# Performance work log

Hardware: AMD Instinct MI355X
Metric: run time of the kernel (lower is better)

Reference implementation:

```python
import jax, jax.numpy as jnp
import numpy as np

H = 16       # num_attention_heads
HKV = 4      # num_key_value_heads
G = H // HKV # num_kv_groups
D = 128      # head_dim
ROT = 64     # rotary dim = head_dim * rope_partial_rotary_factor (0.5)
BLK = 64     # sparse_block_size
LOCAL = 8    # sparse_local_num_blocks
GLOB = 1     # sparse_global_num_blocks
SCALE = 1.0 / float(np.sqrt(D))
NEG = -1000000000.0


def _rotate_half(x):
    x1, x2 = x[..., : x.shape[-1] // 2], x[..., x.shape[-1] // 2 :]
    return jnp.concatenate((-x2, x1), axis=-1)


def _sparse_tables(n_blocks):
    """Static numpy tables mirroring _get_sparse_tables + causal masking.
    Returns idx (n,S) int32 gather table and mask (n, BLK, S, BLK) bool (True = masked)."""
    S = LOCAL + GLOB
    idx = np.zeros((n_blocks, S), np.int32)
    valid = np.zeros((n_blocks, S), bool)
    for i in range(n_blocks):
        sel = [g for g in range(GLOB) if g < n_blocks]
        sel += list(range(max(0, i - (LOCAL - 1)), i + 1))
        li = list(dict.fromkeys(sel))  # dedupe, keep order
        idx[i, : len(li)] = li
        valid[i, : len(li)] = True
    ii = np.arange(n_blocks)[:, None]
    dead = (~valid) | (idx > ii)          # invalid slot or future block
    selfb = idx == ii                     # diagonal block -> intra-causal
    jq = np.arange(BLK)[:, None]
    jk = np.arange(BLK)[None, :]
    intra = jk > jq                       # (q, k) strictly-upper masked
    mask = dead[:, None, :, None] | (selfb[:, None, :, None] & intra[None, :, None, :])
    return idx, mask                      # (n,S), (n,BLK,S,BLK)


def setup_inputs() -> dict:
    key = jax.random.key(0)
    ks = jax.random.split(key, 6)
    B_, T, HID = 2, 4096, 2048
    hidden_states = jax.random.normal(ks[0], (B_, T, HID), dtype=jnp.float32)
    # real RoPE tables for the rotary sub-dim
    inv_freq = 1.0 / (10000.0 ** (np.arange(0, ROT, 2, dtype=np.float32) / ROT))
    freqs = np.arange(T, dtype=np.float32)[:, None] * inv_freq[None, :]
    emb = np.concatenate([freqs, freqs], axis=-1)  # (T, ROT)
    cos = jnp.broadcast_to(jnp.asarray(np.cos(emb)), (B_, T, ROT))
    sin = jnp.broadcast_to(jnp.asarray(np.sin(emb)), (B_, T, ROT))
    Wq = jax.random.normal(ks[1], (H * D, HID), dtype=jnp.float32) * 0.02
    Wk = jax.random.normal(ks[2], (HKV * D, HID), dtype=jnp.float32) * 0.02
    Wv = jax.random.normal(ks[3], (HKV * D, HID), dtype=jnp.float32) * 0.02
    Wo = jax.random.normal(ks[4], (HID, H * D), dtype=jnp.float32) * 0.02
    return {"hidden_states": hidden_states, "cos": cos, "sin": sin,
            "Wq": Wq, "Wk": Wk, "Wv": Wv, "Wo": Wo}


def reference(hidden_states, cos, sin, Wq, Wk, Wv, Wo):
    B_, T, _ = hidden_states.shape
    q = (hidden_states @ Wq.T).reshape(B_, T, H, D).transpose(0, 2, 1, 3)    # (b,H,T,D)
    k = (hidden_states @ Wk.T).reshape(B_, T, HKV, D).transpose(0, 2, 1, 3)  # (b,HKV,T,D)
    v = (hidden_states @ Wv.T).reshape(B_, T, HKV, D).transpose(0, 2, 1, 3)
    # partial RoPE on first ROT dims
    c = cos[:, None, :, :]
    s = sin[:, None, :, :]
    def rope(x):
        xr, xp = x[..., :ROT], x[..., ROT:]
        xr = xr * c + _rotate_half(xr) * s
        return jnp.concatenate([xr, xp], axis=-1)
    q, k = rope(q), rope(k)
    # block-sparse local+global attention (prefill, T multiple of BLK)
    n = T // BLK
    idx_np, mask_np = _sparse_tables(n)
    idx = jnp.asarray(idx_np)
    mask = jnp.asarray(mask_np)  # (n, BLKq, S, BLKk)
    qb = q.reshape(B_, HKV, G, n, BLK, D)
    kb = k.reshape(B_, HKV, n, BLK, D)
    vb = v.reshape(B_, HKV, n, BLK, D)
    ksel = kb[:, :, idx]  # (b,HKV,n,S,BLK,D)
    vsel = vb[:, :, idx]
    scores = jnp.einsum('bhgnqd,bhnskd->bhgnqsk',
                        qb.astype(jnp.float32), ksel.astype(jnp.float32)) * SCALE
    scores = jnp.where(mask[None, None, None], NEG, scores)
    sh = scores.shape
    probs = jax.nn.softmax(scores.reshape(*sh[:5], -1), axis=-1).reshape(sh)
    out = jnp.einsum('bhgnqsk,bhnskd->bhgnqd', probs, vsel.astype(jnp.float32))
    out = out.astype(hidden_states.dtype).reshape(B_, H, T, D)
    out = out.transpose(0, 2, 1, 3).reshape(B_, T, H * D)
    return out @ Wo.T
```

## Files before the change

### kernel.cpp

```cpp
#include <hip/hip_runtime.h>
#include <hip/hip_bf16.h>

#define Hq   16
#define HKV  4
#define Dh   128
#define ROT  64
#define BLKQ 64
#define NBLK 64
#define Tlen 4096
#define Bsz  2
#define HID  2048
#define QKVC 3072
#define SCALE_C 0.08838834764831845f

typedef __attribute__((ext_vector_type(8))) short bf16x8;
typedef __attribute__((ext_vector_type(4))) float f32x4;

#define MFMA16(a, b, c) __builtin_amdgcn_mfma_f32_16x16x32_bf16((a), (b), (c), 0, 0, 0)

__device__ __forceinline__ void async_copy16(__hip_bfloat16* lds, const __hip_bfloat16* g) {
    __builtin_amdgcn_global_load_lds(
        (const __attribute__((address_space(1))) void*)g,
        (__attribute__((address_space(3))) void*)lds,
        16, 0, 0);
}

__global__ __launch_bounds__(256) void cvt_kernel(
    const float* __restrict__ s0, const float* __restrict__ s1,
    const float* __restrict__ s2, const float* __restrict__ s3,
    const float* __restrict__ s4,
    __hip_bfloat16* __restrict__ base,
    int n0, int n1, int n2, int n3, int n4)
{
    const float* src;
    size_t off, n;
    switch (blockIdx.y) {
        case 0:  src = s0; off = 0;                          n = n0; break;
        case 1:  src = s1; off = (size_t)n0;                 n = n1; break;
        case 2:  src = s2; off = (size_t)n0 + n1;            n = n2; break;
        case 3:  src = s3; off = (size_t)n0 + n1 + n2;       n = n3; break;
        default: src = s4; off = (size_t)n0 + n1 + n2 + n3;  n = n4; break;
    }
    __hip_bfloat16* dst = base + off;
    const size_t stride = (size_t)gridDim.x * 2048;
    for (size_t i = ((size_t)blockIdx.x * 256 + threadIdx.x) * 8; i < n; i += stride) {
        const float4 a = *(const float4*)(src + i);
        const float4 b = *(const float4*)(src + i + 4);
        union { bf16x8 v; __hip_bfloat16 e[8]; } u;
        u.e[0] = __float2bfloat16(a.x); u.e[1] = __float2bfloat16(a.y);
        u.e[2] = __float2bfloat16(a.z); u.e[3] = __float2bfloat16(a.w);
        u.e[4] = __float2bfloat16(b.x); u.e[5] = __float2bfloat16(b.y);
        u.e[6] = __float2bfloat16(b.z); u.e[7] = __float2bfloat16(b.w);
        *(bf16x8*)(dst + i) = u.v;
    }
}

template <bool ROPE_, bool F32OUT>
__global__ __launch_bounds__(256, 2) void gemm128db(
    const __hip_bfloat16* __restrict__ A,
    const __hip_bfloat16* __restrict__ B0,
    const __hip_bfloat16* __restrict__ B1,
    const __hip_bfloat16* __restrict__ B2,
    int n1c, int n2c,
    void* __restrict__ C,
    int M, int N, int K,
    const float* __restrict__ cosb,
    const float* __restrict__ sinb)
{
    __shared__ __align__(16) __hip_bfloat16 As[2][128 * 64];
    __shared__ __align__(16) __hip_bfloat16 Bs[2][128 * 64];

    const int m0 = blockIdx.y * 128;
    const int n0 = blockIdx.x * 128;
    const __hip_bfloat16* Bp;
    int nb;
    if (n0 < n1c)      { Bp = B0; nb = n0; }
    else if (n0 < n2c) { Bp = B1; nb = n0 - n1c; }
    else               { Bp = B2; nb = n0 - n2c; }

    const int tid  = threadIdx.x;
    const int lane = tid & 63;
    const int w    = tid >> 6;
    const int wm   = (w >> 1) * 64;
    const int wn   = (w & 1) * 64;
    const int lr   = lane >> 3;
    const int lc   = lane & 7;
    const int m16  = lane & 15;
    const int q8   = lane >> 4;
    const int NT   = K >> 6;

    f32x4 acc[4][4] = {};

    auto stageA = [&](int buf, int kc) {
        #pragma unroll
        for (int ii = 0; ii < 4; ++ii) {
            const int r8 = w * 32 + ii * 8;
            const int r  = r8 + lr;
            const int cg = lc ^ (r & 7);
            async_copy16(&As[buf][r8 * 64], A + (size_t)(m0 + r) * K + kc + cg * 8);
        }
    };
    auto stageB = [&](int buf, int kc) {
        #pragma unroll
        for (int ii = 0; ii < 4; ++ii) {
            const int r8 = w * 32 + ii * 8;
            const int r  = r8 + lr;
            const int cg = lc ^ (r & 7);
            async_copy16(&Bs[buf][r8 * 64], Bp + (size_t)(nb + r) * K + kc + cg * 8);
        }
    };

    stageA(0, 0);
    stageB(0, 0);
    stageA(1, 64);
    stageB(1, 64);
    asm volatile("s_waitcnt vmcnt(8)" ::: "memory");
    __builtin_amdgcn_s_barrier();

    for (int u = 0; u < NT; ++u) {
        const int P  = u & 1;
        const __hip_bfloat16* Ap_ = As[P];
        const __hip_bfloat16* Bq_ = Bs[P];

        bf16x8 a0[4], b0[4], a1[4], b1[4];
        #pragma unroll
        for (int t = 0; t < 4; ++t) {
            const int row = wm + t * 16 + m16;
            const int col = wn + t * 16 + m16;
            a0[t] = *(const bf16x8*)&Ap_[row * 64 + ((q8)     ^ (row & 7)) * 8];
            b0[t] = *(const bf16x8*)&Bq_[col * 64 + ((q8)     ^ (col & 7)) * 8];
            a1[t] = *(const bf16x8*)&Ap_[row * 64 + ((4 + q8) ^ (row & 7)) * 8];
            b1[t] = *(const bf16x8*)&Bq_[col * 64 + ((4 + q8) ^ (col & 7)) * 8];
        }
        asm volatile("s_waitcnt lgkmcnt(0)" ::: "memory");
        __builtin_amdgcn_sched_barrier(0);
        __builtin_amdgcn_s_barrier();
        __builtin_amdgcn_sched_barrier(0);

        if (u + 2 < NT) {
            stageA(P, (u + 2) << 6);
            stageB(P, (u + 2) << 6);
        }

        __builtin_amdgcn_s_setprio(1);
        #pragma unroll
        for (int i = 0; i < 4; ++i)
            #pragma unroll
            for (int j = 0; j < 4; ++j)
                acc[i][j] = MFMA16(a0[i], b0[j], acc[i][j]);
        #pragma unroll
        for (int i = 0; i < 4; ++i)
            #pragma unroll
            for (int j = 0; j < 4; ++j)
                acc[i][j] = MFMA16(a1[i], b1[j], acc[i][j]);
        __builtin_amdgcn_s_setprio(0);

        if (u + 2 < NT) {
            asm volatile("s_waitcnt vmcnt(8)" ::: "memory");
        } else {
            asm volatile("s_waitcnt vmcnt(0)" ::: "memory");
        }
        __builtin_amdgcn_s_barrier();
    }

    if (ROPE_ && n0 < n2c && wn == 0) {
        #pragma unroll
        for (int i = 0; i < 4; ++i)
            #pragma unroll
            for (int r = 0; r < 4; ++r) {
                const int bt = m0 + wm + i * 16 + q8 * 4 + r;
                #pragma unroll
                for (int j = 0; j < 2; ++j) {
                    const int d = j * 16 + m16;
                    const float c = cosb[(size_t)bt * ROT + d];
                    const float s = sinb[(size_t)bt * ROT + d];
                    const float x1 = acc[i][j][r];
                    const float x2 = acc[i][j + 2][r];
                    acc[i][j][r]     = x1 * c - x2 * s;
                    acc[i][j + 2][r] = x2 * c + x1 * s;
                }
            }
    }

    #pragma unroll
    for (int i = 0; i < 4; ++i)
        #pragma unroll
        for (int j = 0; j < 4; ++j)
            #pragma unroll
            for (int r = 0; r < 4; ++r) {
                const int row = m0 + wm + i * 16 + q8 * 4 + r;
                const int col = n0 + wn + j * 16 + m16;
                if (F32OUT)
                    ((float*)C)[(size_t)row * N + col] = acc[i][j][r];
                else
                    ((__hip_bfloat16*)C)[(size_t)row * N + col] =
                        __float2bfloat16(acc[i][j][r]);
            }
}

__global__ __launch_bounds__(256) void vtrans_kernel(
    const __hip_bfloat16* __restrict__ qkv,
    __hip_bfloat16* __restrict__ vtg)
{
    const int tb = blockIdx.x;
    const int pr = blockIdx.y;
    const __hip_bfloat16* src =
        qkv + ((size_t)(pr >> 2) * Tlen + tb * 64) * QKVC + HID + 512 + (pr & 3) * Dh;
    __hip_bfloat16* dst = vtg + (size_t)pr * Dh * Tlen + tb * 64;
    const int tid = threadIdx.x;
    #pragma unroll
    for (int t2 = 0; t2 < 4; ++t2) {
        const int c  = tid + t2 * 256;
        const int d  = c >> 3;
        const int t0 = (c & 7) * 8;
        union { bf16x8 v; __hip_bfloat16 e[8]; } u;
        #pragma unroll
        for (int j = 0; j < 8; ++j)
            u.e[j] = src[(size_t)(t0 + j) * QKVC + d];
        *(bf16x8*)(dst + (size_t)d * Tlen + t0) = u.v;
    }
}

__global__ __launch_bounds__(256, 3) void attn_kernel(
    const __hip_bfloat16* __restrict__ qkv,
    const __hip_bfloat16* __restrict__ vtg,
    __hip_bfloat16* __restrict__ outb)
{
    const int i   = blockIdx.x;
    const int h   = blockIdx.y;
    const int b   = blockIdx.z;
    const int kvh = h >> 2;
    const int tid  = threadIdx.x;
    const int lane = tid & 63;
    const int w    = tid >> 6;
    const int m16  = lane & 15;
    const int q8   = lane >> 4;

    __shared__ __align__(16) __hip_bfloat16 Ks[64 * 136];
    __shared__ __align__(16) __hip_bfloat16 VT[128 * 72];
    __shared__ __align__(16) __hip_bfloat16 Pb[4][16 * 72];

    bf16x8 qf[4];
    {
        const __hip_bfloat16* qp =
            qkv + (size_t)(b * Tlen + i * BLKQ + w * 16 + m16) * QKVC + h * Dh + q8 * 8;
        for (int ks = 0; ks < 4; ++ks) qf[ks] = *(const bf16x8*)(qp + ks * 32);
    }

    f32x4 o[8] = {};
    float mrow[4] = {-1e30f, -1e30f, -1e30f, -1e30f};
    float lrow[4] = {0.f, 0.f, 0.f, 0.f};

    const int nsel = (i + 1 < 9) ? (i + 1) : 9;
    auto kb_of = [&](int j) { return (i <= 7) ? j : ((j == 0) ? 0 : (i - 8 + j)); };

    const __hip_bfloat16* vtbase = vtg + (size_t)(b * HKV + kvh) * Dh * Tlen;

    bf16x8 kr[4], vr[4];
    {
        const int kb0 = kb_of(0);
        const __hip_bfloat16* kbase =
            qkv + (size_t)(b * Tlen + kb0 * BLKQ) * QKVC + HID + kvh * Dh;
        #pragma unroll
        for (int t = 0; t < 4; ++t) {
            const int c = tid + t * 256;
            kr[t] = *(const bf16x8*)(kbase + (size_t)(c >> 4) * QKVC + (c & 15) * 8);
            vr[t] = *(const bf16x8*)(vtbase + (size_t)(c >> 3) * Tlen
                                     + kb0 * BLKQ + (c & 7) * 8);
        }
    }

    for (int j = 0; j < nsel; ++j) {
        const int kb = kb_of(j);

        __syncthreads();
        #pragma unroll
        for (int t = 0; t < 4; ++t) {
            const int c = tid + t * 256;
            *(bf16x8*)&Ks[(c >> 4) * 136 + (c & 15) * 8] = kr[t];
        }
        #pragma unroll
        for (int t = 0; t < 4; ++t) {
            const int c = tid + t * 256;
            *(bf16x8*)&VT[(c >> 3) * 72 + (c & 7) * 8] = vr[t];
        }
        __syncthreads();

        if (j + 1 < nsel) {
            const int kbn = kb_of(j + 1);
            const __hip_bfloat16* kbase =
                qkv + (size_t)(b * Tlen + kbn * BLKQ) * QKVC + HID + kvh * Dh;
            #pragma unroll
            for (int t = 0; t < 4; ++t) {
                const int c = tid + t * 256;
                kr[t] = *(const bf16x8*)(kbase + (size_t)(c >> 4) * QKVC + (c & 15) * 8);
                vr[t] = *(const bf16x8*)(vtbase + (size_t)(c >> 3) * Tlen
                                         + kbn * BLKQ + (c & 7) * 8);
            }
        }

        float sv[4][4];
        __builtin_amdgcn_s_setprio(1);
        for (int nt = 0; nt < 4; ++nt) {
            f32x4 s = {0.f, 0.f, 0.f, 0.f};
            for (int ks = 0; ks < 4; ++ks) {
                bf16x8 kf = *(const bf16x8*)&Ks[(nt * 16 + m16) * 136 + ks * 32 + q8 * 8];
                s = MFMA16(qf[ks], kf, s);
            }
            for (int r = 0; r < 4; ++r) sv[nt][r] = s[r] * SCALE_C;
        }
        __builtin_amdgcn_s_setprio(0);
        if (kb == i) {
            for (int nt = 0; nt < 4; ++nt) {
                const int key = nt * 16 + m16;
                for (int r = 0; r < 4; ++r) {
                    const int qr = w * 16 + q8 * 4 + r;
                    if (key > qr) sv[nt][r] = -1e9f;
                }
            }
        }

        float alpha[4];
        for (int r = 0; r < 4; ++r) {
            float mx = fmaxf(fmaxf(sv[0][r], sv[1][r]), fmaxf(sv[2][r], sv[3][r]));
            for (int off = 1; off < 16; off <<= 1) mx = fmaxf(mx, __shfl_xor(mx, off, 64));
            const float newm = fmaxf(mrow[r], mx);
            alpha[r] = __expf(mrow[r] - newm);
            mrow[r] = newm;
            float rs = 0.f;
            for (int nt = 0; nt < 4; ++nt) {
                const float p = __expf(sv[nt][r] - newm);
                sv[nt][r] = p;
                rs += p;
            }
            for (int off = 1; off < 16; off <<= 1) rs += __shfl_xor(rs, off, 64);
            lrow[r] = lrow[r] * alpha[r] + rs;
        }

        __hip_bfloat16* Pw = &Pb[w][0];
        for (int nt = 0; nt < 4; ++nt)
            for (int r = 0; r < 4; ++r)
                Pw[(q8 * 4 + r) * 72 + nt * 16 + m16] = __float2bfloat16(sv[nt][r]);

        for (int dt = 0; dt < 8; ++dt)
            for (int r = 0; r < 4; ++r)
                o[dt][r] *= alpha[r];

        asm volatile("s_waitcnt lgkmcnt(0)" ::: "memory");
        __builtin_amdgcn_sched_barrier(0);

        __builtin_amdgcn_s_setprio(1);
        for (int kk = 0; kk < 2; ++kk) {
            bf16x8 pf = *(const bf16x8*)&Pw[m16 * 72 + kk * 32 + q8 * 8];
            for (int dt = 0; dt < 8; ++dt) {
                bf16x8 vf = *(const bf16x8*)&VT[(dt * 16 + m16) * 72 + kk * 32 + q8 * 8];
                o[dt] = MFMA16(pf, vf, o[dt]);
            }
        }
        __builtin_amdgcn_s_setprio(0);
    }

    float rcp[4];
    for (int r = 0; r < 4; ++r) rcp[r] = 1.0f / lrow[r];
    __hip_bfloat16* op = outb + (size_t)(b * Tlen + i * BLKQ) * (Hq * Dh) + h * Dh;
    for (int dt = 0; dt < 8; ++dt)
        for (int r = 0; r < 4; ++r) {
            const float val = o[dt][r] * rcp[r];
            op[(size_t)(w * 16 + q8 * 4 + r) * (Hq * Dh) + dt * 16 + m16] =
                __float2bfloat16(val);
        }
}

extern "C" void kernel_launch(void* const* d_in, const int* in_sizes, int n_in,
                              void* d_out, int out_size, void* d_ws, size_t ws_size,
                              hipStream_t stream) {
    const float* hs   = (const float*)d_in[0];
    const float* cosb = (const float*)d_in[1];
    const float* sinb = (const float*)d_in[2];
    const float* Wq   = (const float*)d_in[3];
    const float* Wk   = (const float*)d_in[4];
    const float* Wv   = (const float*)d_in[5];
    const float* Wo   = (const float*)d_in[6];

    const int M = Bsz * Tlen;
    const int nHS = M * HID;
    const int nWq = Hq * Dh * HID;
    const int nWk = HKV * Dh * HID;
    const int nWv = nWk;
    const int nWo = HID * Hq * Dh;

    __hip_bfloat16* hsb  = (__hip_bfloat16*)d_ws;
    __hip_bfloat16* wqb  = hsb + nHS;
    __hip_bfloat16* wkb  = wqb + nWq;
    __hip_bfloat16* wvb  = wkb + nWk;
    __hip_bfloat16* wob  = wvb + nWv;
    __hip_bfloat16* qkv  = wob + nWo;
    __hip_bfloat16* attn = qkv + (size_t)M * QKVC;
    __hip_bfloat16* vtg  = attn + (size_t)M * (Hq * Dh);

    cvt_kernel<<<dim3(8192, 5), 256, 0, stream>>>(
        hs, Wq, Wk, Wv, Wo, hsb, nHS, nWq, nWk, nWv, nWo);
    gemm128db<true, false><<<dim3(QKVC / 128, M / 128), 256, 0, stream>>>(
        hsb, wqb, wkb, wvb, HID, HID + 512, qkv, M, QKVC, HID, cosb, sinb);
    vtrans_kernel<<<dim3(NBLK, Bsz * HKV), 256, 0, stream>>>(qkv, vtg);
    attn_kernel<<<dim3(NBLK, Hq, Bsz), 256, 0, stream>>>(qkv, vtg, attn);
    gemm128db<false, true><<<dim3(HID / 128, M / 128), 256, 0, stream>>>(
        attn, wob, wob, wob, HID, HID, d_out, M, HID, HID, nullptr, nullptr);
}
```

Baseline: 415.8 us.

## Transpose attention MFMA operands so each lane owns one query row

Swaps the A/B operands of both MFMAs so the accumulator is transposed. Each lane now holds a single query row, which cuts the softmax max and sum reductions from four 16-lane shuffle trees to two shuffles per row. P is written to LDS as packed 4-element vectors and the output as 8-byte stores. VT and P tiles switch from padded rows to an XOR-swizzled layout to avoid bank conflicts without padding. This reduces shuffle and LDS traffic, with some risk of a wrong swizzle or layout mismatch.

Measured after the change: 413.6 us. Within noise of the previous version (-0.5%).

```diff
diff --git a/kernel.cpp b/kernel.cpp
--- a/kernel.cpp
+++ b/kernel.cpp
@@ -15,6 +15,7 @@
 
 typedef __attribute__((ext_vector_type(8))) short bf16x8;
 typedef __attribute__((ext_vector_type(4))) float f32x4;
+typedef __attribute__((ext_vector_type(4))) unsigned short u16x4;
 
 #define MFMA16(a, b, c) __builtin_amdgcn_mfma_f32_16x16x32_bf16((a), (b), (c), 0, 0, 0)
 
@@ -237,8 +238,8 @@
     const int q8   = lane >> 4;
 
     __shared__ __align__(16) __hip_bfloat16 Ks[64 * 136];
-    __shared__ __align__(16) __hip_bfloat16 VT[128 * 72];
-    __shared__ __align__(16) __hip_bfloat16 Pb[4][16 * 72];
+    __shared__ __align__(16) __hip_bfloat16 VT[128 * 64];
+    __shared__ __align__(16) __hip_bfloat16 Pb[4][16 * 64];
 
     bf16x8 qf[4];
     {
@@ -248,8 +249,7 @@
     }
 
     f32x4 o[8] = {};
-    float mrow[4] = {-1e30f, -1e30f, -1e30f, -1e30f};
-    float lrow[4] = {0.f, 0.f, 0.f, 0.f};
+    float mrow = -1e30f, lrow = 0.f;
 
     const int nsel = (i + 1 < 9) ? (i + 1) : 9;
     auto kb_of = [&](int j) { return (i <= 7) ? j : ((j == 0) ? 0 : (i - 8 + j)); };
@@ -282,7 +282,8 @@
         #pragma unroll
         for (int t = 0; t < 4; ++t) {
             const int c = tid + t * 256;
-            *(bf16x8*)&VT[(c >> 3) * 72 + (c & 7) * 8] = vr[t];
+            const int row = c >> 3;
+            *(bf16x8*)&VT[row * 64 + (((c & 7) ^ (row & 7)) << 3)] = vr[t];
         }
         __syncthreads();
 
@@ -305,70 +306,88 @@
             f32x4 s = {0.f, 0.f, 0.f, 0.f};
             for (int ks = 0; ks < 4; ++ks) {
                 bf16x8 kf = *(const bf16x8*)&Ks[(nt * 16 + m16) * 136 + ks * 32 + q8 * 8];
-                s = MFMA16(qf[ks], kf, s);
+                s = MFMA16(kf, qf[ks], s);
             }
             for (int r = 0; r < 4; ++r) sv[nt][r] = s[r] * SCALE_C;
         }
         __builtin_amdgcn_s_setprio(0);
         if (kb == i) {
-            for (int nt = 0; nt < 4; ++nt) {
-                const int key = nt * 16 + m16;
-                for (int r = 0; r < 4; ++r) {
-                    const int qr = w * 16 + q8 * 4 + r;
-                    if (key > qr) sv[nt][r] = -1e9f;
-                }
-            }
-        }
-
-        float alpha[4];
-        for (int r = 0; r < 4; ++r) {
-            float mx = fmaxf(fmaxf(sv[0][r], sv[1][r]), fmaxf(sv[2][r], sv[3][r]));
-            for (int off = 1; off < 16; off <<= 1) mx = fmaxf(mx, __shfl_xor(mx, off, 64));
-            const float newm = fmaxf(mrow[r], mx);
-            alpha[r] = __expf(mrow[r] - newm);
-            mrow[r] = newm;
-            float rs = 0.f;
-            for (int nt = 0; nt < 4; ++nt) {
+            const int qr = w * 16 + m16;
+            #pragma unroll
+            for (int nt = 0; nt < 4; ++nt)
+                #pragma unroll
+                for (int r = 0; r < 4; ++r)
+                    if (nt * 16 + q8 * 4 + r > qr) sv[nt][r] = -1e9f;
+        }
+
+        float mx = sv[0][0];
+        #pragma unroll
+        for (int nt = 0; nt < 4; ++nt)
+            #pragma unroll
+            for (int r = 0; r < 4; ++r) mx = fmaxf(mx, sv[nt][r]);
+        mx = fmaxf(mx, __shfl_xor(mx, 16, 64));
+        mx = fmaxf(mx, __shfl_xor(mx, 32, 64));
+        const float newm = fmaxf(mrow, mx);
+        const float alpha = __expf(mrow - newm);
+        mrow = newm;
+        float rs = 0.f;
+        #pragma unroll
+        for (int nt = 0; nt < 4; ++nt)
+            #pragma unroll
+            for (int r = 0; r < 4; ++r) {
                 const float p = __expf(sv[nt][r] - newm);
                 sv[nt][r] = p;
                 rs += p;
             }
-            for (int off = 1; off < 16; off <<= 1) rs += __shfl_xor(rs, off, 64);
-            lrow[r] = lrow[r] * alpha[r] + rs;
-        }
+        rs += __shfl_xor(rs, 16, 64);
+        rs += __shfl_xor(rs, 32, 64);
+        lrow = lrow * alpha + rs;
 
         __hip_bfloat16* Pw = &Pb[w][0];
-        for (int nt = 0; nt < 4; ++nt)
+        #pragma unroll
+        for (int nt = 0; nt < 4; ++nt) {
+            union { u16x4 v; __hip_bfloat16 e[4]; } u;
+            u.e[0] = __float2bfloat16(sv[nt][0]);
+            u.e[1] = __float2bfloat16(sv[nt][1]);
+            u.e[2] = __float2bfloat16(sv[nt][2]);
+            u.e[3] = __float2bfloat16(sv[nt][3]);
+            const int chunk = (nt * 2 + (q8 >> 1)) ^ (m16 & 7);
+            *(u16x4*)&Pw[m16 * 64 + (chunk << 3) + ((q8 & 1) << 2)] = u.v;
+        }
+
+        #pragma unroll
+        for (int dt = 0; dt < 8; ++dt)
+            #pragma unroll
             for (int r = 0; r < 4; ++r)
-                Pw[(q8 * 4 + r) * 72 + nt * 16 + m16] = __float2bfloat16(sv[nt][r]);
-
-        for (int dt = 0; dt < 8; ++dt)
-            for (int r = 0; r < 4; ++r)
-                o[dt][r] *= alpha[r];
+                o[dt][r] *= alpha;
 
         asm volatile("s_waitcnt lgkmcnt(0)" ::: "memory");
         __builtin_amdgcn_sched_barrier(0);
 
         __builtin_amdgcn_s_setprio(1);
         for (int kk = 0; kk < 2; ++kk) {
-            bf16x8 pf = *(const bf16x8*)&Pw[m16 * 72 + kk * 32 + q8 * 8];
+            const int co = ((kk * 4 + q8) ^ (m16 & 7)) << 3;
+            bf16x8 pf = *(const bf16x8*)&Pw[m16 * 64 + co];
+            #pragma unroll
             for (int dt = 0; dt < 8; ++dt) {
-                bf16x8 vf = *(const bf16x8*)&VT[(dt * 16 + m16) * 72 + kk * 32 + q8 * 8];
-                o[dt] = MFMA16(pf, vf, o[dt]);
+                bf16x8 vf = *(const bf16x8*)&VT[(dt * 16 + m16) * 64 + co];
+                o[dt] = MFMA16(vf, pf, o[dt]);
             }
         }
         __builtin_amdgcn_s_setprio(0);
     }
 
-    float rcp[4];
-    for (int r = 0; r < 4; ++r) rcp[r] = 1.0f / lrow[r];
-    __hip_bfloat16* op = outb + (size_t)(b * Tlen + i * BLKQ) * (Hq * Dh) + h * Dh;
-    for (int dt = 0; dt < 8; ++dt)
-        for (int r = 0; r < 4; ++r) {
-            const float val = o[dt][r] * rcp[r];
-            op[(size_t)(w * 16 + q8 * 4 + r) * (Hq * Dh) + dt * 16 + m16] =
-                __float2bfloat16(val);
-        }
+    const float rcp = 1.0f / lrow;
+    __hip_bfloat16* op = outb + (size_t)(b * Tlen + i * BLKQ + w * 16 + m16) * (Hq * Dh)
+                        + h * Dh + q8 * 4;
+    #pragma unroll
+    for (int dt = 0; dt < 8; ++dt) {
+        union { u16x4 v; __hip_bfloat16 e[4]; } u;
+        #pragma unroll
+        for (int r = 0; r < 4; ++r)
+            u.e[r] = __float2bfloat16(o[dt][r] * rcp);
+        *(u16x4*)(op + dt * 16) = u.v;
+    }
 }
 
 extern "C" void kernel_launch(void* const* d_in, const int* in_sizes, int n_in,
```
